# Kernel tuning notes

Hardware: AMD Instinct MI355X
Metric: run time of the kernel (lower is better)

The kernel has to match this reference:

```python
import jax, jax.numpy as jnp
import numpy as np
from jax import lax

B, C_IN, T = 64, 40, 8192

def conv1d(x, w, b):
    # x: [B,C,T], w: [O,I,K] (torch Conv1d layout), stride 2, VALID padding
    y = lax.conv_general_dilated(x, w, window_strides=(2,), padding='VALID',
                                 dimension_numbers=('NCH', 'OIH', 'NCH'))
    return y + b[None, :, None]

def avgpool2(x):
    # AvgPool1d(kernel=2, stride=2): pairwise mean, drop trailing odd element
    t2 = x.shape[-1] // 2
    return x[..., :2 * t2].reshape(x.shape[0], x.shape[1], t2, 2).mean(-1)

def setup_inputs():
    key = jax.random.key(0)
    ks = jax.random.split(key, 24)
    def w_init(k, shape, fan_in):
        return jax.random.normal(k, shape, jnp.float32) * (1.0 / np.sqrt(fan_in))
    inp = {}
    inp['x_input'] = jax.random.normal(ks[0], (B, C_IN, T), jnp.float32)
    # per-sample valid lengths in [2048, 8192] so the deep strided stack leaves >=1 frame
    inp['len_mask'] = 2048 + jax.random.randint(ks[1], (B,), 0, T - 2048 + 1, dtype=jnp.int32)
    convs = [(96, C_IN, 10), (96, 96, 5), (96, 96, 5), (96, 96, 5), (96, 96, 5), (96, 96, 5), (128, 96, 3)]
    for i, (o, ci, k) in enumerate(convs):
        inp[f'w{i+1}'] = w_init(ks[2 + 2 * i], (o, ci, k), ci * k)
        inp[f'b{i+1}'] = jnp.zeros((o,), jnp.float32)
    lins = [(128, 128), (64, 128), (5, 64)]
    for i, (o, ci) in enumerate(lins):
        inp[f'lw{i+1}'] = w_init(ks[16 + 2 * i], (o, ci), ci)
        inp[f'lb{i+1}'] = jnp.zeros((o,), jnp.float32)
    return inp

def reference(x_input, len_mask, w1, b1, w2, b2, w3, b3, w4, b4, w5, b5, w6, b6, w7, b7,
              lw1, lb1, lw2, lb2, lw3, lb3):
    # Batched masked equivalent of the per-sample ragged loop: for VALID stride-2 convs,
    # output position j depends only on inputs < valid length when j < valid out-length,
    # so we run batched convs on padded input and track per-sample valid lengths.
    Lv = len_mask.astype(jnp.int32)
    x = jax.nn.relu(conv1d(x_input, w1, b1)); Lv = (Lv - 10) // 2 + 1
    x = jax.nn.relu(conv1d(x, w2, b2));       Lv = (Lv - 5) // 2 + 1
    x = jax.nn.relu(conv1d(x, w3, b3));       Lv = (Lv - 5) // 2 + 1
    # cnn_1d_top (dropout in eval mode = identity)
    x = conv1d(x, w4, b4);        Lv = (Lv - 5) // 2 + 1
    x = jax.nn.relu(avgpool2(x)); Lv = Lv // 2
    x = conv1d(x, w5, b5);        Lv = (Lv - 5) // 2 + 1
    x = jax.nn.relu(avgpool2(x)); Lv = Lv // 2
    x = jax.nn.relu(conv1d(x, w6, b6)); Lv = (Lv - 5) // 2 + 1
    x = jax.nn.relu(conv1d(x, w7, b7)); Lv = (Lv - 3) // 2 + 1
    # AdaptiveMaxPool1d(1) over each sample's valid region
    mask = jnp.arange(x.shape[-1])[None, :] < Lv[:, None]          # [B, T_out]
    x = jnp.max(jnp.where(mask[:, None, :], x, -jnp.inf), axis=-1)  # [B, 128]
    # out1_top MLP head
    h = jax.nn.relu(x @ lw1.T + lb1)
    h = jax.nn.relu(h @ lw2.T + lb2)
    return h @ lw3.T + lb3
```

## Files before the change

### kernel.cpp

```cpp
#include <hip/hip_runtime.h>
#include <hip/hip_bf16.h>
#include <math.h>


typedef __attribute__((ext_vector_type(8))) _Float16 f16x8;
typedef __attribute__((ext_vector_type(4))) float f32x4;

__device__ __forceinline__ unsigned short f2h_bits(float f) {
    union { _Float16 h; unsigned short u; } cv;
    cv.h = (_Float16)f;
    return cv.u;
}

template<int KEFF, int CI, int NBLK, bool IN_FP32, bool RELU, bool OUT_F16,
         bool POOL, int PIPE, int PHASES>
__global__ __launch_bounds__(512, 2)
void conv_nb(const unsigned short* __restrict__ xh,
             const unsigned short* __restrict__ wpk,
             const float* __restrict__ bias,
             unsigned short* __restrict__ yh,
             float* __restrict__ yf,
             int Tin, int Tout)
{
    constexpr int CO    = 96;
    constexpr int NTHR  = 512;
    constexpr int GTOT  = CI * KEFF;
    constexpr int STEPS = (GTOT + 31) / 32;
    constexpr int SH    = STEPS / PHASES;
    constexpr int CIH   = CI / PHASES;
    constexpr int RD    = NBLK + KEFF / 2;
    constexpr int NTW   = NBLK / 64;
    constexpr int TOTH  = CIH * RD;
    constexpr int NIT   = (TOTH + NTHR - 1) / NTHR;
    constexpr int PH    = (32 % KEFF == 0) ? 1 : (((32 * 3) % KEFF == 0) ? 3 : 5);
    constexpr int PERRD = (32 * PH / KEFF) * RD;

    __shared__ unsigned int Bs[TOTH];

    const int tid  = threadIdx.x;
    const int lane = tid & 63;
    const int wave = tid >> 6;
    const int mg   = wave & 1;
    const int tg   = wave >> 1;
    const int quad = lane >> 4;
    const int l16  = lane & 15;
    const int wc0  = tg * (NBLK / 4);

    const int nT = (Tout + NBLK - 1) / NBLK;
    const int b  = blockIdx.x / nT;
    const int t0 = (blockIdx.x % nT) * NBLK;

    const float* xf = (const float*)xh;
    const unsigned int* xb = (const unsigned int*)xh + (((size_t)b * CI * Tin) >> 1);
    const int rowd = Tin >> 1;

    auto stageB = [&](int ph) {
        const int ci0 = ph * CIH;
        #pragma unroll
        for (int it = 0; it < NIT; ++it) {
            int i = tid + it * NTHR;
            if (i < TOTH) {
                int r = (unsigned)i / (unsigned)RD, d = i - r * RD;
                unsigned int v;
                if (IN_FP32) {
                    int e = 2 * (t0 + d);
                    if (e > Tin - 2) e = Tin - 2;
                    const float* src = xf + ((size_t)b * CI + ci0 + r) * Tin + e;
                    float2 w = *(const float2*)src;
                    v = (unsigned int)f2h_bits(w.x) | ((unsigned int)f2h_bits(w.y) << 16);
                } else {
                    int dd = t0 + d;
                    if (dd > rowd - 1) dd = rowd - 1;
                    v = *(xb + (size_t)(ci0 + r) * rowd + dd);
                }
                Bs[i] = v;
            }
        }
    };

    int offb[PH][4];
    #pragma unroll
    for (int ph = 0; ph < PH; ++ph)
        #pragma unroll
        for (int p = 0; p < 4; ++p) {
            int g = 32 * ph + quad * 8 + 2 * p;
            unsigned ci = (unsigned)g / (unsigned)KEFF;
            unsigned dwo = ((unsigned)g - ci * (unsigned)KEFF) >> 1;
            offb[ph][p] = (int)ci * RD + wc0 + l16 + (int)dwo;
        }

    f32x4 acc[3][NTW];
    #pragma unroll
    for (int mt = 0; mt < 3; ++mt)
        #pragma unroll
        for (int nt = 0; nt < NTW; ++nt) acc[mt][nt] = (f32x4)0.f;

    union BvU { unsigned int u[4]; f16x8 v; };

    auto load_step = [&](int sg, int sl, BvU (&Bv)[NTW], f16x8 (&Ah)[3], f16x8 (&Al)[3]) {
        if (32 * (sg + 1) <= GTOT) {
            #pragma unroll
            for (int nt = 0; nt < NTW; ++nt)
                #pragma unroll
                for (int p = 0; p < 4; ++p)
                    Bv[nt].u[p] = Bs[offb[sl % PH][p] + (sl / PH) * PERRD + nt * 16];
        } else {
            #pragma unroll
            for (int nt = 0; nt < NTW; ++nt)
                #pragma unroll
                for (int p = 0; p < 4; ++p) {
                    int g = 32 * sg + quad * 8 + 2 * p;
                    if (g > GTOT - 2) g = GTOT - 2;
                    unsigned ci = (unsigned)g / (unsigned)KEFF;
                    unsigned dwo = ((unsigned)g - ci * (unsigned)KEFF) >> 1;
                    Bv[nt].u[p] = Bs[(int)ci * RD + wc0 + l16 + (int)dwo + nt * 16];
                }
        }
        const unsigned short* ap = wpk + (size_t)sg * 6144 + (size_t)(mg * 3) * 512
                                 + (size_t)lane * 8;
        #pragma unroll
        for (int mt = 0; mt < 3; ++mt) {
            Ah[mt] = *(const f16x8*)(ap + mt * 512);
            Al[mt] = *(const f16x8*)(ap + 3072 + mt * 512);
        }
    };
    auto mfma_step = [&](BvU (&Bv)[NTW], f16x8 (&Ah)[3], f16x8 (&Al)[3]) {
        #pragma unroll
        for (int mt = 0; mt < 3; ++mt)
            #pragma unroll
            for (int nt = 0; nt < NTW; ++nt)
                acc[mt][nt] = __builtin_amdgcn_mfma_f32_16x16x32_f16(Ah[mt], Bv[nt].v, acc[mt][nt], 0, 0, 0);
        #pragma unroll
        for (int mt = 0; mt < 3; ++mt)
            #pragma unroll
            for (int nt = 0; nt < NTW; ++nt)
                acc[mt][nt] = __builtin_amdgcn_mfma_f32_16x16x32_f16(Al[mt], Bv[nt].v, acc[mt][nt], 0, 0, 0);
    };

    #pragma unroll
    for (int ph2 = 0; ph2 < PHASES; ++ph2) {
        if (ph2 > 0) __syncthreads();
        stageB(ph2);
        __syncthreads();

        if (PIPE == 0) {
            #pragma unroll
            for (int s2 = 0; s2 < SH; ++s2) {
                BvU Bv[NTW];
                f16x8 Ah[3], Al[3];
                load_step(ph2 * SH + s2, s2, Bv, Ah, Al);
                mfma_step(Bv, Ah, Al);
            }
        } else {
            BvU  Bv0[NTW], Bv1[NTW];
            f16x8 Ah0[3], Al0[3], Ah1[3], Al1[3];

            load_step(ph2 * SH, 0, Bv0, Ah0, Al0);
            #pragma unroll
            for (int s2 = 0; s2 < SH; ++s2) {
                if (s2 + 1 < SH) {
                    if (((s2 + 1) & 1) == 0) load_step(ph2 * SH + s2 + 1, s2 + 1, Bv0, Ah0, Al0);
                    else                     load_step(ph2 * SH + s2 + 1, s2 + 1, Bv1, Ah1, Al1);
                }
                __builtin_amdgcn_sched_barrier(0);
                __builtin_amdgcn_s_setprio(1);
                if ((s2 & 1) == 0) mfma_step(Bv0, Ah0, Al0);
                else               mfma_step(Bv1, Ah1, Al1);
                __builtin_amdgcn_s_setprio(0);
                __builtin_amdgcn_sched_barrier(0);
            }
        }
    }

    #pragma unroll
    for (int mt = 0; mt < 3; ++mt) {
        #pragma unroll
        for (int r = 0; r < 4; ++r) {
            int o = (mg * 3 + mt) * 16 + quad * 4 + r;
            float bv = bias[o];
            #pragma unroll
            for (int nt = 0; nt < NTW; ++nt) {
                int t = t0 + wc0 + nt * 16 + l16;
                float v = acc[mt][nt][r] + bv;
                if (RELU) v = fmaxf(v, 0.f);
                if (POOL) {
                    float sum = v + __shfl_xor(v, 1, 64);
                    if ((lane & 1) == 0 && t + 1 < Tout) {
                        float pr = fmaxf(0.5f * sum, 0.f);
                        size_t pidx = ((size_t)b * CO + o) * (Tout >> 1) + (t >> 1);
                        if (OUT_F16) yh[pidx] = f2h_bits(pr);
                        else         yf[pidx] = pr;
                    }
                } else if (OUT_F16) {
                    unsigned int h = f2h_bits(v);
                    unsigned int hp = (unsigned int)__shfl_xor((int)h, 1, 64);
                    if ((lane & 1) == 0 && t + 1 < Tout) {
                        size_t base = ((size_t)b * CO + o) * Tout + t;
                        *(unsigned int*)(yh + base) = h | (hp << 16);
                    }
                } else if (t < Tout) {
                    yf[((size_t)b * CO + o) * Tout + t] = v;
                }
            }
        }
    }
}

__device__ __forceinline__ void repack_img(const float* __restrict__ w,
                                           unsigned short* __restrict__ wpk,
                                           int idx, int KP, int KW, int CI)
{
    int j = idx & 7, lane = (idx >> 3) & 63, g = idx >> 9;
    int c = g / 24, r = g % 24;
    int mt = r % 6, sh = r / 6;
    int half = sh & 1, s = sh >> 1;
    int S  = c * 2 + s;
    int kg = S * 32 + (lane >> 4) * 8 + j;
    int o  = mt * 16 + (lane & 15);
    int ci = kg / KP, k = kg - ci * KP;
    float val = (ci < CI && k < KW) ? w[((size_t)o * CI + ci) * KW + k] : 0.f;
    _Float16 hh = (_Float16)val;
    union { _Float16 h; unsigned short u; } cv;
    cv.h = (half == 0) ? hh : (_Float16)(val - (float)hh);
    wpk[idx] = cv.u;
}
__device__ __forceinline__ void repack_okc(const float* __restrict__ w,
                                           float* __restrict__ wr,
                                           int idx, int CI, int K, int CO)
{
    int o = idx % CO; int rem = idx / CO; int k = rem % K; int ci = rem / K;
    wr[idx] = w[((size_t)o * CI + ci) * K + k];
}

__global__ void repack_all(const float* w1, const float* w2, const float* w3,
                           const float* w4, const float* w5, const float* w6,
                           const float* w7,
                           unsigned short* p1, unsigned short* p2,
                           unsigned short* p3, unsigned short* p4,
                           unsigned short* p5, float* r6, float* r7)
{
    int idx = blockIdx.x * 256 + threadIdx.x;
    if (idx < 79872)  { repack_img(w1, p1, idx, 10, 10, 40); return; }
    idx -= 79872;
    if (idx < 110592) { repack_img(w2, p2, idx, 6, 5, 96); return; }
    idx -= 110592;
    if (idx < 110592) { repack_img(w3, p3, idx, 6, 5, 96); return; }
    idx -= 110592;
    if (idx < 110592) { repack_img(w4, p4, idx, 6, 5, 96); return; }
    idx -= 110592;
    if (idx < 110592) { repack_img(w5, p5, idx, 6, 5, 96); return; }
    idx -= 110592;
    if (idx < 46080)  { repack_okc(w6, r6, idx, 96, 5, 96); return; }
    idx -= 46080;
    if (idx < 36864)  { repack_okc(w7, r7, idx, 96, 3, 128); return; }
}

__global__ __launch_bounds__(256)
void conv6_k(const float* __restrict__ y5p, const float* __restrict__ w6r,
             const float* __restrict__ b6, float* __restrict__ y6)
{
    __shared__ float s5[96 * 62];
    const int b = blockIdx.x >> 2, ob = blockIdx.x & 3;
    const int tid = threadIdx.x;
    for (int i = tid; i < 96 * 62; i += 256) s5[i] = y5p[(size_t)b * 96 * 62 + i];
    __syncthreads();

    const int wave = __builtin_amdgcn_readfirstlane(tid >> 6);
    const int t = tid & 63;
    if (t < 29) {
        const int o0 = ob * 24 + wave * 6;
        float a[6];
        #pragma unroll
        for (int oo = 0; oo < 6; oo++) a[oo] = 0.f;
        for (int ci = 0; ci < 96; ci++) {
            float xr[5];
            #pragma unroll
            for (int k = 0; k < 5; k++) xr[k] = s5[ci * 62 + 2 * t + k];
            #pragma unroll
            for (int k = 0; k < 5; k++) {
                const float* wp = w6r + (ci * 5 + k) * 96 + o0;
                #pragma unroll
                for (int oo = 0; oo < 6; oo++)
                    a[oo] = fmaf(wp[oo], xr[k], a[oo]);
            }
        }
        #pragma unroll
        for (int oo = 0; oo < 6; oo++)
            y6[((size_t)b * 96 + o0 + oo) * 29 + t] = fmaxf(a[oo] + b6[o0 + oo], 0.f);
    }
}

__global__ __launch_bounds__(256)
void tail2(const float* __restrict__ y6,
           const float* __restrict__ w7r, const float* __restrict__ b7,
           const int* __restrict__ lens,
           const float* __restrict__ lw1, const float* __restrict__ lb1,
           const float* __restrict__ lw2, const float* __restrict__ lb2,
           const float* __restrict__ lw3, const float* __restrict__ lb3,
           float* __restrict__ out)
{
    __shared__ float s6[96 * 29 + 8];
    __shared__ float s7[128 * 14];
    __shared__ float feat[128], h1[128], h2[64];

    const int b = blockIdx.x, tid = threadIdx.x;
    for (int i = tid; i < 96 * 29; i += 256) s6[i] = y6[(size_t)b * 96 * 29 + i];
    __syncthreads();

    const int wave = __builtin_amdgcn_readfirstlane(tid >> 6);
    const int lane = tid & 63;
    const int sub  = lane >> 4;
    const int tl   = lane & 15;
    {
        float a[32];
        #pragma unroll
        for (int oo = 0; oo < 32; oo++) a[oo] = 0.f;
        const int ci0 = sub * 24;
        for (int ci = ci0; ci < ci0 + 24; ci++) {
            float xr[3];
            #pragma unroll
            for (int k = 0; k < 3; k++) xr[k] = s6[ci * 29 + 2 * tl + k];
            #pragma unroll
            for (int k = 0; k < 3; k++) {
                const float* wp = w7r + (ci * 3 + k) * 128 + wave * 32;
                #pragma unroll
                for (int oo = 0; oo < 32; oo++)
                    a[oo] = fmaf(wp[oo], xr[k], a[oo]);
            }
        }
        #pragma unroll
        for (int oo = 0; oo < 32; oo++) {
            float v = a[oo];
            v += __shfl_xor(v, 16, 64);
            v += __shfl_xor(v, 32, 64);
            if (sub == 0 && tl < 14) {
                int o = wave * 32 + oo;
                s7[o * 14 + tl] = fmaxf(v + b7[o], 0.f);
            }
        }
    }
    __syncthreads();

    if (tid < 128) {
        int L = lens[b];
        L = (L - 10) / 2 + 1;
        L = (L - 5) / 2 + 1;
        L = (L - 5) / 2 + 1;
        L = (L - 5) / 2 + 1;
        L = L / 2;
        L = (L - 5) / 2 + 1;
        L = L / 2;
        L = (L - 5) / 2 + 1;
        L = (L - 3) / 2 + 1;
        float m = -INFINITY;
        for (int t = 0; t < L; t++) m = fmaxf(m, s7[tid * 14 + t]);
        feat[tid] = m;
    }
    __syncthreads();

    if (tid < 128) {
        float s = lb1[tid];
        for (int i = 0; i < 128; i++) s = fmaf(lw1[tid * 128 + i], feat[i], s);
        h1[tid] = fmaxf(s, 0.f);
    }
    __syncthreads();
    if (tid < 64) {
        float s = lb2[tid];
        for (int i = 0; i < 128; i++) s = fmaf(lw2[tid * 128 + i], h1[i], s);
        h2[tid] = fmaxf(s, 0.f);
    }
    __syncthreads();
    if (tid < 5) {
        float s = lb3[tid];
        for (int i = 0; i < 64; i++) s = fmaf(lw3[tid * 64 + i], h2[i], s);
        out[b * 5 + tid] = s;
    }
}

extern "C" void kernel_launch(void* const* d_in, const int* in_sizes, int n_in,
                              void* d_out, int out_size, void* d_ws, size_t ws_size,
                              hipStream_t stream)
{
    const float* x    = (const float*)d_in[0];
    const int*   lens = (const int*)  d_in[1];
    const float* w1 = (const float*)d_in[2];   const float* b1 = (const float*)d_in[3];
    const float* w2 = (const float*)d_in[4];   const float* b2 = (const float*)d_in[5];
    const float* w3 = (const float*)d_in[6];   const float* b3 = (const float*)d_in[7];
    const float* w4 = (const float*)d_in[8];   const float* b4 = (const float*)d_in[9];
    const float* w5 = (const float*)d_in[10];  const float* b5 = (const float*)d_in[11];
    const float* w6 = (const float*)d_in[12];  const float* b6 = (const float*)d_in[13];
    const float* w7 = (const float*)d_in[14];  const float* b7 = (const float*)d_in[15];
    const float* lw1 = (const float*)d_in[16]; const float* lb1 = (const float*)d_in[17];
    const float* lw2 = (const float*)d_in[18]; const float* lb2 = (const float*)d_in[19];
    const float* lw3 = (const float*)d_in[20]; const float* lb3 = (const float*)d_in[21];
    float* out = (float*)d_out;
    char*  W   = (char*)d_ws;

    size_t off = 0;
    auto take = [&](size_t bytes) {
        size_t o = off; off = (off + bytes + 255) & ~(size_t)255; return o;
    };
    size_t o_y3h = take(((size_t)64 * 96 * 1020 + 2048) * 2);
    size_t o_y4h = take(((size_t)64 * 96 * 254 + 2048) * 2);
    size_t o_y5p = take((size_t)64 * 96 * 62 * 4 + 1024);
    size_t o_y6  = take((size_t)64 * 96 * 29 * 4);
    size_t o_wp1 = take((size_t)79872 * 2);
    size_t o_wp2 = take((size_t)110592 * 2);
    size_t o_wp3 = take((size_t)110592 * 2);
    size_t o_wp4 = take((size_t)110592 * 2);
    size_t o_wp5 = take((size_t)110592 * 2);
    size_t o_w6r = take((size_t)46080 * 4);
    size_t o_w7r = take((size_t)36864 * 4);
    size_t persist = off;

    auto chunk_bytes = [&](int Bc) -> size_t {
        size_t s = 0;
        s += ((size_t)Bc * 96 * 4092 + 2048) * 2 + 256;
        s += ((size_t)Bc * 96 * 2044 + 2048) * 2 + 256;
        return s;
    };
    int Bc = 64;
    while (Bc > 1 && persist + chunk_bytes(Bc) > ws_size) Bc >>= 1;
    size_t o_y1h = take(((size_t)Bc * 96 * 4092 + 2048) * 2);
    size_t o_y2h = take(((size_t)Bc * 96 * 2044 + 2048) * 2);

    auto US = [&](size_t o) { return (unsigned short*)(W + o); };
    auto FP = [&](size_t o) { return (float*)(W + o); };

    repack_all<<<dim3((605184 + 255) / 256), 256, 0, stream>>>(
        w1, w2, w3, w4, w5, w6, w7,
        US(o_wp1), US(o_wp2), US(o_wp3), US(o_wp4), US(o_wp5),
        FP(o_w6r), FP(o_w7r));

    const int nchunks = 64 / Bc;
    for (int c = 0; c < nchunks; c++) {
        const float* xc = x + (size_t)c * Bc * 40 * 8192;

        conv_nb<10, 40, 256, true, true, true, false, 0, 1><<<dim3(Bc * 16), 512, 0, stream>>>(
            (const unsigned short*)xc, US(o_wp1), b1, US(o_y1h), nullptr, 8192, 4092);
        conv_nb< 6, 96, 256, false, true, true, false, 0, 2><<<dim3(Bc * 8), 512, 0, stream>>>(
            US(o_y1h), US(o_wp2), b2, US(o_y2h), nullptr, 4092, 2044);
        unsigned short* y3h_c = US(o_y3h) + (size_t)c * Bc * 96 * 1020;
        conv_nb< 6, 96, 128, false, true, true, false, 1, 1><<<dim3(Bc * 8), 512, 0, stream>>>(
            US(o_y2h), US(o_wp3), b3, y3h_c, nullptr, 2044, 1020);
    }

    conv_nb<6, 96, 64, false, false, true, true, 1, 1><<<dim3(64 * 8), 512, 0, stream>>>(
        US(o_y3h), US(o_wp4), b4, US(o_y4h), nullptr, 1020, 508);

    conv_nb<6, 96, 64, false, false, false, true, 1, 1><<<dim3(64 * 2), 512, 0, stream>>>(
        US(o_y4h), US(o_wp5), b5, nullptr, FP(o_y5p), 254, 125);

    conv6_k<<<dim3(256), 256, 0, stream>>>(FP(o_y5p), FP(o_w6r), b6, FP(o_y6));

    tail2<<<dim3(64), 256, 0, stream>>>(
        FP(o_y6), FP(o_w7r), b7, lens, lw1, lb1, lw2, lb2, lw3, lb3, out);
}
```

Before: 384.0 us.

## Fuse conv5, conv6, conv7 and MLP head into one per-sample tail kernel

Replaces the conv5 launch, the conv6 kernel and the tail kernel with a single kernel per batch sample. It computes conv5 with split-f16 MFMA from shared memory, then pools and runs conv6, conv7, the masked max and the MLP entirely in LDS. This removes two launches and the global round trips for the y5 and y6 intermediates. It also retunes conv2 to a 128-wide block with the pipelined variant and twice the grid. The cost is that the fused tail runs only 64 blocks, so much of the GPU sits idle during that stage.

```diff
diff --git a/kernel.cpp b/kernel.cpp
--- a/kernel.cpp
+++ b/kernel.cpp
@@ -206,6 +206,231 @@
     }
 }
 
+__global__ __launch_bounds__(512, 2)
+void tail3(const unsigned short* __restrict__ y4h,
+           const unsigned short* __restrict__ wpk5,
+           const float* __restrict__ b5,
+           const float* __restrict__ w6r, const float* __restrict__ b6,
+           const float* __restrict__ w7r, const float* __restrict__ b7,
+           const int* __restrict__ lens,
+           const float* __restrict__ lw1, const float* __restrict__ lb1,
+           const float* __restrict__ lw2, const float* __restrict__ lb2,
+           const float* __restrict__ lw3, const float* __restrict__ lb3,
+           float* __restrict__ out)
+{
+    constexpr int RD  = 131;
+    constexpr int TOT = 96 * RD;
+    constexpr int NIT = (TOT + 511) / 512;
+    constexpr int PERRD = 16 * RD;
+
+    __shared__ __align__(16) unsigned int smem[TOT];
+    float* const y5s  = (float*)smem;
+    float* const y6s  = (float*)smem + 96 * 62;
+    float* const s7   = (float*)smem + 96 * 62 + 96 * 29 + 8;
+    float* const feat = s7 + 128 * 14;
+    float* const h1   = feat + 128;
+    float* const h2   = h1 + 128;
+
+    const int tid  = threadIdx.x;
+    const int lane = tid & 63;
+    const int wave = tid >> 6;
+    const int mg   = wave & 1;
+    const int tg   = wave >> 1;
+    const int quad = lane >> 4;
+    const int l16  = lane & 15;
+    const int wc0  = tg * 32;
+    const int b    = blockIdx.x;
+
+    const unsigned int* xb = (const unsigned int*)y4h + (size_t)b * 96 * 127;
+    #pragma unroll
+    for (int it = 0; it < NIT; ++it) {
+        int i = tid + it * 512;
+        if (i < TOT) {
+            int r = (unsigned)i / (unsigned)RD, d = i - r * RD;
+            if (d > 126) d = 126;
+            smem[i] = xb[(size_t)r * 127 + d];
+        }
+    }
+    __syncthreads();
+
+    int offb[3][4];
+    #pragma unroll
+    for (int ph = 0; ph < 3; ++ph)
+        #pragma unroll
+        for (int p = 0; p < 4; ++p) {
+            int g = 32 * ph + quad * 8 + 2 * p;
+            int ci = g / 6, dwo = (g - ci * 6) >> 1;
+            offb[ph][p] = ci * RD + wc0 + l16 + dwo;
+        }
+
+    f32x4 acc[3][2];
+    #pragma unroll
+    for (int mt = 0; mt < 3; ++mt)
+        #pragma unroll
+        for (int nt = 0; nt < 2; ++nt) acc[mt][nt] = (f32x4)0.f;
+
+    union BvU { unsigned int u[4]; f16x8 v; };
+    auto load_step = [&](int s, BvU (&Bv)[2], f16x8 (&Ah)[3], f16x8 (&Al)[3]) {
+        #pragma unroll
+        for (int nt = 0; nt < 2; ++nt)
+            #pragma unroll
+            for (int p = 0; p < 4; ++p)
+                Bv[nt].u[p] = smem[offb[s % 3][p] + (s / 3) * PERRD + nt * 16];
+        const unsigned short* ap = wpk5 + (size_t)s * 6144 + (size_t)(mg * 3) * 512
+                                 + (size_t)lane * 8;
+        #pragma unroll
+        for (int mt = 0; mt < 3; ++mt) {
+            Ah[mt] = *(const f16x8*)(ap + mt * 512);
+            Al[mt] = *(const f16x8*)(ap + 3072 + mt * 512);
+        }
+    };
+    auto mfma_step = [&](BvU (&Bv)[2], f16x8 (&Ah)[3], f16x8 (&Al)[3]) {
+        #pragma unroll
+        for (int mt = 0; mt < 3; ++mt)
+            #pragma unroll
+            for (int nt = 0; nt < 2; ++nt)
+                acc[mt][nt] = __builtin_amdgcn_mfma_f32_16x16x32_f16(Ah[mt], Bv[nt].v, acc[mt][nt], 0, 0, 0);
+        #pragma unroll
+        for (int mt = 0; mt < 3; ++mt)
+            #pragma unroll
+            for (int nt = 0; nt < 2; ++nt)
+                acc[mt][nt] = __builtin_amdgcn_mfma_f32_16x16x32_f16(Al[mt], Bv[nt].v, acc[mt][nt], 0, 0, 0);
+    };
+
+    {
+        BvU  Bv0[2], Bv1[2];
+        f16x8 Ah0[3], Al0[3], Ah1[3], Al1[3];
+        load_step(0, Bv0, Ah0, Al0);
+        #pragma unroll
+        for (int s = 0; s < 18; ++s) {
+            if (s + 1 < 18) {
+                if (((s + 1) & 1) == 0) load_step(s + 1, Bv0, Ah0, Al0);
+                else                    load_step(s + 1, Bv1, Ah1, Al1);
+            }
+            __builtin_amdgcn_sched_barrier(0);
+            __builtin_amdgcn_s_setprio(1);
+            if ((s & 1) == 0) mfma_step(Bv0, Ah0, Al0);
+            else              mfma_step(Bv1, Ah1, Al1);
+            __builtin_amdgcn_s_setprio(0);
+            __builtin_amdgcn_sched_barrier(0);
+        }
+    }
+
+    __syncthreads();
+
+    #pragma unroll
+    for (int mt = 0; mt < 3; ++mt) {
+        #pragma unroll
+        for (int r = 0; r < 4; ++r) {
+            int o = (mg * 3 + mt) * 16 + quad * 4 + r;
+            float bv = b5[o];
+            #pragma unroll
+            for (int nt = 0; nt < 2; ++nt) {
+                int t = wc0 + nt * 16 + l16;
+                float v = acc[mt][nt][r] + bv;
+                float sum = v + __shfl_xor(v, 1, 64);
+                if ((lane & 1) == 0 && t + 1 < 125)
+                    y5s[o * 62 + (t >> 1)] = fmaxf(0.5f * sum, 0.f);
+            }
+        }
+    }
+    __syncthreads();
+
+    {
+        const int half = lane >> 5;
+        const int t = lane & 31;
+        const int o0 = wave * 12 + half * 6;
+        if (t < 29) {
+            float a6[6];
+            #pragma unroll
+            for (int oo = 0; oo < 6; oo++) a6[oo] = 0.f;
+            for (int ci = 0; ci < 96; ci++) {
+                float xr[5];
+                #pragma unroll
+                for (int k = 0; k < 5; k++) xr[k] = y5s[ci * 62 + 2 * t + k];
+                #pragma unroll
+                for (int k = 0; k < 5; k++) {
+                    const float* wp = w6r + (ci * 5 + k) * 96 + o0;
+                    #pragma unroll
+                    for (int oo = 0; oo < 6; oo++)
+                        a6[oo] = fmaf(wp[oo], xr[k], a6[oo]);
+                }
+            }
+            #pragma unroll
+            for (int oo = 0; oo < 6; oo++)
+                y6s[(o0 + oo) * 29 + t] = fmaxf(a6[oo] + b6[o0 + oo], 0.f);
+        }
+    }
+    __syncthreads();
+
+    {
+        const int sub = lane >> 4;
+        const int tl  = lane & 15;
+        float a7[16];
+        #pragma unroll
+        for (int oo = 0; oo < 16; oo++) a7[oo] = 0.f;
+        const int ci0 = sub * 24;
+        for (int ci = ci0; ci < ci0 + 24; ci++) {
+            float xr[3];
+            #pragma unroll
+            for (int k = 0; k < 3; k++) xr[k] = y6s[ci * 29 + 2 * tl + k];
+            #pragma unroll
+            for (int k = 0; k < 3; k++) {
+                const float* wp = w7r + (ci * 3 + k) * 128 + wave * 16;
+                #pragma unroll
+                for (int oo = 0; oo < 16; oo++)
+                    a7[oo] = fmaf(wp[oo], xr[k], a7[oo]);
+            }
+        }
+        #pragma unroll
+        for (int oo = 0; oo < 16; oo++) {
+            float v = a7[oo];
+            v += __shfl_xor(v, 16, 64);
+            v += __shfl_xor(v, 32, 64);
+            if (sub == 0 && tl < 14) {
+                int o = wave * 16 + oo;
+                s7[o * 14 + tl] = fmaxf(v + b7[o], 0.f);
+            }
+        }
+    }
+    __syncthreads();
+
+    if (tid < 128) {
+        int L = lens[b];
+        L = (L - 10) / 2 + 1;
+        L = (L - 5) / 2 + 1;
+        L = (L - 5) / 2 + 1;
+        L = (L - 5) / 2 + 1;
+        L = L / 2;
+        L = (L - 5) / 2 + 1;
+        L = L / 2;
+        L = (L - 5) / 2 + 1;
+        L = (L - 3) / 2 + 1;
+        float m = -INFINITY;
+        for (int t = 0; t < L; t++) m = fmaxf(m, s7[tid * 14 + t]);
+        feat[tid] = m;
+    }
+    __syncthreads();
+
+    if (tid < 128) {
+        float s = lb1[tid];
+        for (int i = 0; i < 128; i++) s = fmaf(lw1[tid * 128 + i], feat[i], s);
+        h1[tid] = fmaxf(s, 0.f);
+    }
+    __syncthreads();
+    if (tid < 64) {
+        float s = lb2[tid];
+        for (int i = 0; i < 128; i++) s = fmaf(lw2[tid * 128 + i], h1[i], s);
+        h2[tid] = fmaxf(s, 0.f);
+    }
+    __syncthreads();
+    if (tid < 5) {
+        float s = lb3[tid];
+        for (int i = 0; i < 64; i++) s = fmaf(lw3[tid * 64 + i], h2[i], s);
+        out[b * 5 + tid] = s;
+    }
+}
+
 __device__ __forceinline__ void repack_img(const float* __restrict__ w,
                                            unsigned short* __restrict__ wpk,
                                            int idx, int KP, int KW, int CI)
@@ -255,128 +480,6 @@
     if (idx < 36864)  { repack_okc(w7, r7, idx, 96, 3, 128); return; }
 }
 
-__global__ __launch_bounds__(256)
-void conv6_k(const float* __restrict__ y5p, const float* __restrict__ w6r,
-             const float* __restrict__ b6, float* __restrict__ y6)
-{
-    __shared__ float s5[96 * 62];
-    const int b = blockIdx.x >> 2, ob = blockIdx.x & 3;
-    const int tid = threadIdx.x;
-    for (int i = tid; i < 96 * 62; i += 256) s5[i] = y5p[(size_t)b * 96 * 62 + i];
-    __syncthreads();
-
-    const int wave = __builtin_amdgcn_readfirstlane(tid >> 6);
-    const int t = tid & 63;
-    if (t < 29) {
-        const int o0 = ob * 24 + wave * 6;
-        float a[6];
-        #pragma unroll
-        for (int oo = 0; oo < 6; oo++) a[oo] = 0.f;
-        for (int ci = 0; ci < 96; ci++) {
-            float xr[5];
-            #pragma unroll
-            for (int k = 0; k < 5; k++) xr[k] = s5[ci * 62 + 2 * t + k];
-            #pragma unroll
-            for (int k = 0; k < 5; k++) {
-                const float* wp = w6r + (ci * 5 + k) * 96 + o0;
-                #pragma unroll
-                for (int oo = 0; oo < 6; oo++)
-                    a[oo] = fmaf(wp[oo], xr[k], a[oo]);
-            }
-        }
-        #pragma unroll
-        for (int oo = 0; oo < 6; oo++)
-            y6[((size_t)b * 96 + o0 + oo) * 29 + t] = fmaxf(a[oo] + b6[o0 + oo], 0.f);
-    }
-}
-
-__global__ __launch_bounds__(256)
-void tail2(const float* __restrict__ y6,
-           const float* __restrict__ w7r, const float* __restrict__ b7,
-           const int* __restrict__ lens,
-           const float* __restrict__ lw1, const float* __restrict__ lb1,
-           const float* __restrict__ lw2, const float* __restrict__ lb2,
-           const float* __restrict__ lw3, const float* __restrict__ lb3,
-           float* __restrict__ out)
-{
-    __shared__ float s6[96 * 29 + 8];
-    __shared__ float s7[128 * 14];
-    __shared__ float feat[128], h1[128], h2[64];
-
-    const int b = blockIdx.x, tid = threadIdx.x;
-    for (int i = tid; i < 96 * 29; i += 256) s6[i] = y6[(size_t)b * 96 * 29 + i];
-    __syncthreads();
-
-    const int wave = __builtin_amdgcn_readfirstlane(tid >> 6);
-    const int lane = tid & 63;
-    const int sub  = lane >> 4;
-    const int tl   = lane & 15;
-    {
-        float a[32];
-        #pragma unroll
-        for (int oo = 0; oo < 32; oo++) a[oo] = 0.f;
-        const int ci0 = sub * 24;
-        for (int ci = ci0; ci < ci0 + 24; ci++) {
-            float xr[3];
-            #pragma unroll
-            for (int k = 0; k < 3; k++) xr[k] = s6[ci * 29 + 2 * tl + k];
-            #pragma unroll
-            for (int k = 0; k < 3; k++) {
-                const float* wp = w7r + (ci * 3 + k) * 128 + wave * 32;
-                #pragma unroll
-                for (int oo = 0; oo < 32; oo++)
-                    a[oo] = fmaf(wp[oo], xr[k], a[oo]);
-            }
-        }
-        #pragma unroll
-        for (int oo = 0; oo < 32; oo++) {
-            float v = a[oo];
-            v += __shfl_xor(v, 16, 64);
-            v += __shfl_xor(v, 32, 64);
-            if (sub == 0 && tl < 14) {
-                int o = wave * 32 + oo;
-                s7[o * 14 + tl] = fmaxf(v + b7[o], 0.f);
-            }
-        }
-    }
-    __syncthreads();
-
-    if (tid < 128) {
-        int L = lens[b];
-        L = (L - 10) / 2 + 1;
-        L = (L - 5) / 2 + 1;
-        L = (L - 5) / 2 + 1;
-        L = (L - 5) / 2 + 1;
-        L = L / 2;
-        L = (L - 5) / 2 + 1;
-        L = L / 2;
-        L = (L - 5) / 2 + 1;
-        L = (L - 3) / 2 + 1;
-        float m = -INFINITY;
-        for (int t = 0; t < L; t++) m = fmaxf(m, s7[tid * 14 + t]);
-        feat[tid] = m;
-    }
-    __syncthreads();
-
-    if (tid < 128) {
-        float s = lb1[tid];
-        for (int i = 0; i < 128; i++) s = fmaf(lw1[tid * 128 + i], feat[i], s);
-        h1[tid] = fmaxf(s, 0.f);
-    }
-    __syncthreads();
-    if (tid < 64) {
-        float s = lb2[tid];
-        for (int i = 0; i < 128; i++) s = fmaf(lw2[tid * 128 + i], h1[i], s);
-        h2[tid] = fmaxf(s, 0.f);
-    }
-    __syncthreads();
-    if (tid < 5) {
-        float s = lb3[tid];
-        for (int i = 0; i < 64; i++) s = fmaf(lw3[tid * 64 + i], h2[i], s);
-        out[b * 5 + tid] = s;
-    }
-}
-
 extern "C" void kernel_launch(void* const* d_in, const int* in_sizes, int n_in,
                               void* d_out, int out_size, void* d_ws, size_t ws_size,
                               hipStream_t stream)
@@ -402,8 +505,6 @@
     };
     size_t o_y3h = take(((size_t)64 * 96 * 1020 + 2048) * 2);
     size_t o_y4h = take(((size_t)64 * 96 * 254 + 2048) * 2);
-    size_t o_y5p = take((size_t)64 * 96 * 62 * 4 + 1024);
-    size_t o_y6  = take((size_t)64 * 96 * 29 * 4);
     size_t o_wp1 = take((size_t)79872 * 2);
     size_t o_wp2 = take((size_t)110592 * 2);
     size_t o_wp3 = take((size_t)110592 * 2);
@@ -438,7 +539,7 @@
 
         conv_nb<10, 40, 256, true, true, true, false, 0, 1><<<dim3(Bc * 16), 512, 0, stream>>>(
             (const unsigned short*)xc, US(o_wp1), b1, US(o_y1h), nullptr, 8192, 4092);
-        conv_nb< 6, 96, 256, false, true, true, false, 0, 2><<<dim3(Bc * 8), 512, 0, stream>>>(
+        conv_nb< 6, 96, 128, false, true, true, false, 1, 1><<<dim3(Bc * 16), 512, 0, stream>>>(
             US(o_y1h), US(o_wp2), b2, US(o_y2h), nullptr, 4092, 2044);
         unsigned short* y3h_c = US(o_y3h) + (size_t)c * Bc * 96 * 1020;
         conv_nb< 6, 96, 128, false, true, true, false, 1, 1><<<dim3(Bc * 8), 512, 0, stream>>>(
@@ -448,11 +549,7 @@
     conv_nb<6, 96, 64, false, false, true, true, 1, 1><<<dim3(64 * 8), 512, 0, stream>>>(
         US(o_y3h), US(o_wp4), b4, US(o_y4h), nullptr, 1020, 508);
 
-    conv_nb<6, 96, 64, false, false, false, true, 1, 1><<<dim3(64 * 2), 512, 0, stream>>>(
-        US(o_y4h), US(o_wp5), b5, nullptr, FP(o_y5p), 254, 125);
-
-    conv6_k<<<dim3(256), 256, 0, stream>>>(FP(o_y5p), FP(o_w6r), b6, FP(o_y6));
-
-    tail2<<<dim3(64), 256, 0, stream>>>(
-        FP(o_y6), FP(o_w7r), b7, lens, lw1, lb1, lw2, lb2, lw3, lb3, out);
-}
+    tail3<<<dim3(64), 512, 0, stream>>>(
+        US(o_y4h), US(o_wp5), b5, FP(o_w6r), b6, FP(o_w7r), b7,
+        lens, lw1, lb1, lw2, lb2, lw3, lb3, out);
+}
```

Measured after the change: 386.3 us. No clear change (+0.6%).
